# Kernel tuning notes

Measured on AMD Instinct MI355X. Metric: run time of the kernel, lower is better.

The kernel has to match this reference:

```python
import jax, jax.numpy as jnp
import numpy as np

N_NODES = 50000
SEQ = 12
CH = 128
BS = 4

def setup_inputs() -> dict:
    key = jax.random.key(0)
    k1, k2, k3, k4, k5 = jax.random.split(key, 5)
    x = jax.random.normal(k1, (BS, N_NODES, CH), dtype=jnp.float32)
    indices = jax.random.randint(k2, (N_NODES, SEQ), 0, N_NODES)
    # xavier-uniform-like init for per-node spiral weights [n_nodes, seq]
    bound = float(np.sqrt(6.0 / (N_NODES + SEQ)))
    weight = jax.random.uniform(k3, (N_NODES, SEQ), minval=-bound, maxval=bound, dtype=jnp.float32)
    gate_w = jax.random.normal(k4, (CH, CH), dtype=jnp.float32) * (1.0 / np.sqrt(CH))
    gate_b = jax.random.normal(k5, (CH,), dtype=jnp.float32) * 0.01
    return {"x": x, "indices": indices, "weight": weight, "gate_w": gate_w, "gate_b": gate_b}

def reference(x, indices, weight, gate_w, gate_b):
    # gate projection: [bs, n, ch]
    gate = jnp.einsum('bnc,dc->bnd', x, gate_w) + gate_b
    # gather spiral neighbors along node axis: [bs, n*s, ch] -> [bs, n, s, ch]
    gathered = jnp.take(x, indices.reshape(-1), axis=1)
    gathered = gathered.reshape(x.shape[0], indices.shape[0], indices.shape[1], x.shape[2])
    # per-node weighted reduction over spiral positions
    out = jnp.einsum('bvsf,vs->bvf', gathered, weight)
    return out * gate
```

## Files before the change

### kernel.cpp

```cpp
#include <hip/hip_runtime.h>
#include <hip/hip_bf16.h>

#define N_NODES 50000
#define SEQ 12
#define CH 128
#define BS 4
#define TILE 64
#define NTILES ((N_NODES + TILE - 1) / TILE)
#define HALF 64
#define PAD_S 68
#define PAD_ROW 132

#define CNODES 4
#define NCHUNK 4
#define CHUNK_SHORTS (CNODES * SEQ * HALF)
#define CHUNK_INSTR (CHUNK_SHORTS / 512)

typedef short bf16x8 __attribute__((ext_vector_type(8)));
typedef float f32x4 __attribute__((ext_vector_type(4)));

__device__ __forceinline__ float bflo(unsigned int u) { return __uint_as_float(u << 16); }
__device__ __forceinline__ float bfhi(unsigned int u) { return __uint_as_float(u & 0xFFFF0000u); }

__device__ __forceinline__ void gload_lds16b(const unsigned short* g, unsigned short* l) {
    __builtin_amdgcn_global_load_lds(
        (const __attribute__((address_space(1))) void*)g,
        (__attribute__((address_space(3))) void*)l,
        16, 0, 0);
}
__device__ __forceinline__ void gload_lds16f(const float* g, float* l) {
    __builtin_amdgcn_global_load_lds(
        (const __attribute__((address_space(1))) void*)g,
        (__attribute__((address_space(3))) void*)l,
        16, 0, 0);
}

__global__ __launch_bounds__(256) void convert_kernel(
    const float* __restrict__ x,
    unsigned short* __restrict__ xb)
{
    const size_t i = (size_t)blockIdx.x * 256 + threadIdx.x;
    const size_t n8 = (size_t)BS * N_NODES * CH / 8;
    if (i < n8) {
        float4 lo = *(const float4*)(x + i * 8);
        float4 hi = *(const float4*)(x + i * 8 + 4);
        union { bf16x8 v; __hip_bfloat16 h[8]; } o;
        o.h[0] = __float2bfloat16(lo.x); o.h[1] = __float2bfloat16(lo.y);
        o.h[2] = __float2bfloat16(lo.z); o.h[3] = __float2bfloat16(lo.w);
        o.h[4] = __float2bfloat16(hi.x); o.h[5] = __float2bfloat16(hi.y);
        o.h[6] = __float2bfloat16(hi.z); o.h[7] = __float2bfloat16(hi.w);
        *(bf16x8*)(xb + i * 8) = o.v;
    }
}

__global__ __launch_bounds__(256, 2) void gated_spiral_slice(
    const unsigned short* __restrict__ xb,
    const int* __restrict__ indices,
    const float* __restrict__ weight,
    const float* __restrict__ gate_w,
    const float* __restrict__ gate_b,
    float* __restrict__ out)
{
    __shared__ float spiral[TILE * PAD_S];
    __shared__ unsigned short gbuf[4][2][CHUNK_SHORTS];
    __shared__ int   idx_s[TILE * SEQ];
    __shared__ float w_s[TILE * SEQ];

    const int tid  = threadIdx.x;
    const int wave = tid >> 6;
    const int lane = tid & 63;

    const int grp  = blockIdx.x & 7;
    const int b    = grp >> 1;
    const int half = grp & 1;
    const int tile = blockIdx.x >> 3;
    const int node0 = tile * TILE;
    const unsigned short* xbb = xb + (size_t)b * N_NODES * CH;

    const int sbase = wave * 16 * SEQ;
    #pragma unroll
    for (int k3 = 0; k3 < 3; ++k3) {
        const int k = k3 * 64 + lane;
        int node = node0 + wave * 16 + k / SEQ;
        if (node >= N_NODES) node = N_NODES - 1;
        int t = indices[(size_t)node * SEQ + (k % SEQ)];
        t = t < 0 ? 0 : (t >= N_NODES ? N_NODES - 1 : t);
        idx_s[sbase + k] = t;
        w_s[sbase + k]   = weight[(size_t)node * SEQ + (k % SEQ)];
    }

    {
        const int* idxw = idx_s + sbase;
        const float* ww = w_s + sbase;
        unsigned short* gw0 = &gbuf[wave][0][0];
        const int lrs = lane >> 3;
        const int lco = (lane & 7) * 8;

        #pragma unroll
        for (int c0 = 0; c0 < 2; ++c0) {
            unsigned short* dst = gw0 + c0 * CHUNK_SHORTS;
            #pragma unroll
            for (int i = 0; i < CHUNK_INSTR; ++i) {
                const int rs = i * 8 + lrs;
                const int s = rs >> 2, n = rs & 3;
                const int row = idxw[(c0 * CNODES + n) * SEQ + s];
                gload_lds16b(xbb + (size_t)row * CH + half * HALF + lco, dst + i * 512);
            }
        }

        #pragma unroll
        for (int c = 0; c < NCHUNK; ++c) {
            if (c < NCHUNK - 1) asm volatile("s_waitcnt vmcnt(6)" ::: "memory");
            else                asm volatile("s_waitcnt vmcnt(0)" ::: "memory");
            __builtin_amdgcn_sched_barrier(0);

            unsigned short* bufp = gw0 + (c & 1) * CHUNK_SHORTS;
            const int nr = lane >> 4;
            const int cc = (lane & 15) * 4;
            const float* wp = ww + (c * CNODES + nr) * SEQ;
            float a0 = 0.f, a1 = 0.f, a2 = 0.f, a3 = 0.f;
            #pragma unroll
            for (int s = 0; s < SEQ; ++s) {
                const uint2 d = *(const uint2*)(bufp + (s * 4 + nr) * HALF + cc);
                const float ws = wp[s];
                a0 += ws * bflo(d.x); a1 += ws * bfhi(d.x);
                a2 += ws * bflo(d.y); a3 += ws * bfhi(d.y);
            }
            const int r = wave * 16 + c * CNODES + nr;
            *(float4*)(spiral + r * PAD_S + cc) = make_float4(a0, a1, a2, a3);

            if (c + 2 < NCHUNK) {
                asm volatile("s_waitcnt lgkmcnt(0)" ::: "memory");
                __builtin_amdgcn_sched_barrier(0);
                #pragma unroll
                for (int i = 0; i < CHUNK_INSTR; ++i) {
                    const int rs = i * 8 + lrs;
                    const int s = rs >> 2, n = rs & 3;
                    const int row = idxw[((c + 2) * CNODES + n) * SEQ + s];
                    gload_lds16b(xbb + (size_t)row * CH + half * HALF + lco, bufp + i * 512);
                }
            }
        }
    }

    {
        const int m = lane & 15;
        const int quad = lane >> 4;

        int arow_node = node0 + wave * 16 + m;
        if (arow_node >= N_NODES) arow_node = N_NODES - 1;
        const unsigned short* ap = xbb + (size_t)arow_node * CH + quad * 8;

        bf16x8 afrag[4];
        #pragma unroll
        for (int kk = 0; kk < 4; ++kk)
            afrag[kk] = *(const bf16x8*)(ap + kk * 32);

        float gbv[4];
        #pragma unroll
        for (int t = 0; t < 4; ++t)
            gbv[t] = gate_b[half * HALF + t * 16 + m];

        #pragma unroll
        for (int t = 0; t < 4; ++t) {
            f32x4 c = {0.f, 0.f, 0.f, 0.f};
            const float* bp = gate_w + (size_t)(half * HALF + t * 16 + m) * CH + quad * 8;
            #pragma unroll
            for (int kk = 0; kk < 4; ++kk) {
                float4 lo = *(const float4*)(bp + kk * 32);
                float4 hi = *(const float4*)(bp + kk * 32 + 4);
                union { bf16x8 v; __hip_bfloat16 h[8]; } bf;
                bf.h[0] = __float2bfloat16(lo.x); bf.h[1] = __float2bfloat16(lo.y);
                bf.h[2] = __float2bfloat16(lo.z); bf.h[3] = __float2bfloat16(lo.w);
                bf.h[4] = __float2bfloat16(hi.x); bf.h[5] = __float2bfloat16(hi.y);
                bf.h[6] = __float2bfloat16(hi.z); bf.h[7] = __float2bfloat16(hi.w);
                c = __builtin_amdgcn_mfma_f32_16x16x32_bf16(afrag[kk], bf.v, c, 0, 0, 0);
            }
            #pragma unroll
            for (int reg = 0; reg < 4; ++reg) {
                const int r = wave * 16 + quad * 4 + reg;
                const int col = t * 16 + m;
                const float sp = spiral[r * PAD_S + col];
                spiral[r * PAD_S + col] = sp * (c[reg] + gbv[t]);
            }
        }
    }

    {
        #pragma unroll
        for (int p = 0; p < 4; ++p) {
            const int seg = p * 64 + lane;
            const int r = seg >> 4;
            const int cc = (seg & 15) * 4;
            const int node = node0 + wave * 16 + r;
            if (node < N_NODES) {
                const float* sp = spiral + (wave * 16 + r) * PAD_S + cc;
                f32x4 v = { sp[0], sp[1], sp[2], sp[3] };
                __builtin_nontemporal_store(v,
                    (f32x4*)(out + ((size_t)b * N_NODES + node) * CH + half * HALF + cc));
            }
        }
    }
}

#define NODES_PER_WAVE 16
#define FCHUNK_NODES 2
#define FCHUNK_FLOATS (FCHUNK_NODES * SEQ * CH)
#define FNCHUNK (NODES_PER_WAVE / FCHUNK_NODES)

__global__ __launch_bounds__(256, 1) void gated_spiral_async(
    const float* __restrict__ x,
    const int* __restrict__ indices,
    const float* __restrict__ weight,
    const float* __restrict__ gate_w,
    const float* __restrict__ gate_b,
    float* __restrict__ out)
{
    __shared__ float spiral[TILE * PAD_ROW];
    __shared__ float gbuf[4][2][FCHUNK_FLOATS];
    __shared__ int   idx_s[TILE * SEQ];
    __shared__ float w_s[TILE * SEQ];

    const int tid  = threadIdx.x;
    const int wave = tid >> 6;
    const int lane = tid & 63;
    const int b    = blockIdx.y;
    const int node0 = blockIdx.x * TILE;
    const float* xb = x + (size_t)b * N_NODES * CH;

    const int sbase = wave * NODES_PER_WAVE * SEQ;
    #pragma unroll
    for (int k3 = 0; k3 < 3; ++k3) {
        const int k = k3 * 64 + lane;
        int node = node0 + wave * NODES_PER_WAVE + k / SEQ;
        if (node >= N_NODES) node = N_NODES - 1;
        int t = indices[(size_t)node * SEQ + (k % SEQ)];
        t = t < 0 ? 0 : (t >= N_NODES ? N_NODES - 1 : t);
        idx_s[sbase + k] = t;
        w_s[sbase + k]   = weight[(size_t)node * SEQ + (k % SEQ)];
    }

    {
        const int n  = lane >> 5;
        const int co = (lane & 31) * 4;
        const int* idxw = idx_s + sbase;
        const float* ww = w_s + sbase;
        float* gb0 = &gbuf[wave][0][0];

        #pragma unroll
        for (int c0 = 0; c0 < 2; ++c0) {
            const int* ix = idxw + c0 * FCHUNK_NODES * SEQ;
            float* dst = gb0 + c0 * FCHUNK_FLOATS;
            #pragma unroll
            for (int s = 0; s < SEQ; ++s) {
                const int row = ix[n * SEQ + s];
                gload_lds16f(xb + (size_t)row * CH + co, dst + s * (FCHUNK_NODES * CH));
            }
        }

        #pragma unroll
        for (int c = 0; c < FNCHUNK; ++c) {
            if (c < FNCHUNK - 1) asm volatile("s_waitcnt vmcnt(12)" ::: "memory");
            else                 asm volatile("s_waitcnt vmcnt(0)"  ::: "memory");
            __builtin_amdgcn_sched_barrier(0);

            float* cur = gb0 + (c & 1) * FCHUNK_FLOATS;
            const float* wp = ww + c * FCHUNK_NODES * SEQ + n * SEQ;
            float a0 = 0.f, a1 = 0.f, a2 = 0.f, a3 = 0.f;
            #pragma unroll
            for (int s = 0; s < SEQ; ++s) {
                const float4 d = *(const float4*)(cur + (s * FCHUNK_NODES + n) * CH + co);
                const float ws = wp[s];
                a0 += ws * d.x; a1 += ws * d.y; a2 += ws * d.z; a3 += ws * d.w;
            }
            const int r = wave * NODES_PER_WAVE + c * FCHUNK_NODES + n;
            *(float4*)(spiral + r * PAD_ROW + co) = make_float4(a0, a1, a2, a3);

            if (c + 2 < FNCHUNK) {
                asm volatile("s_waitcnt lgkmcnt(0)" ::: "memory");
                __builtin_amdgcn_sched_barrier(0);
                const int* ix = idxw + (c + 2) * FCHUNK_NODES * SEQ;
                #pragma unroll
                for (int s = 0; s < SEQ; ++s) {
                    const int row = ix[n * SEQ + s];
                    gload_lds16f(xb + (size_t)row * CH + co, cur + s * (FCHUNK_NODES * CH));
                }
            }
        }
    }

    {
        const int m = lane & 15;
        const int quad = lane >> 4;

        int arow_node = node0 + wave * 16 + m;
        if (arow_node >= N_NODES) arow_node = N_NODES - 1;
        const float* ap = xb + (size_t)arow_node * CH + quad * 8;

        bf16x8 afrag[4];
        #pragma unroll
        for (int kk = 0; kk < 4; ++kk) {
            float4 lo = *(const float4*)(ap + kk * 32);
            float4 hi = *(const float4*)(ap + kk * 32 + 4);
            union { bf16x8 v; __hip_bfloat16 h[8]; } af;
            af.h[0] = __float2bfloat16(lo.x); af.h[1] = __float2bfloat16(lo.y);
            af.h[2] = __float2bfloat16(lo.z); af.h[3] = __float2bfloat16(lo.w);
            af.h[4] = __float2bfloat16(hi.x); af.h[5] = __float2bfloat16(hi.y);
            af.h[6] = __float2bfloat16(hi.z); af.h[7] = __float2bfloat16(hi.w);
            afrag[kk] = af.v;
        }

        float gbv[8];
        #pragma unroll
        for (int t = 0; t < 8; ++t)
            gbv[t] = gate_b[t * 16 + m];

        #pragma unroll
        for (int t = 0; t < 8; ++t) {
            f32x4 c = {0.f, 0.f, 0.f, 0.f};
            const float* bp = gate_w + (size_t)(t * 16 + m) * CH + quad * 8;
            #pragma unroll
            for (int kk = 0; kk < 4; ++kk) {
                float4 lo = *(const float4*)(bp + kk * 32);
                float4 hi = *(const float4*)(bp + kk * 32 + 4);
                union { bf16x8 v; __hip_bfloat16 h[8]; } bf;
                bf.h[0] = __float2bfloat16(lo.x); bf.h[1] = __float2bfloat16(lo.y);
                bf.h[2] = __float2bfloat16(lo.z); bf.h[3] = __float2bfloat16(lo.w);
                bf.h[4] = __float2bfloat16(hi.x); bf.h[5] = __float2bfloat16(hi.y);
                bf.h[6] = __float2bfloat16(hi.z); bf.h[7] = __float2bfloat16(hi.w);
                c = __builtin_amdgcn_mfma_f32_16x16x32_bf16(afrag[kk], bf.v, c, 0, 0, 0);
            }
            #pragma unroll
            for (int reg = 0; reg < 4; ++reg) {
                const int r = wave * 16 + quad * 4 + reg;
                const int col = t * 16 + m;
                const float sp = spiral[r * PAD_ROW + col];
                spiral[r * PAD_ROW + col] = sp * (c[reg] + gbv[t]);
            }
        }
    }

    {
        #pragma unroll
        for (int p = 0; p < 8; ++p) {
            const int seg = p * 64 + lane;
            const int r = seg >> 5;
            const int c4 = (seg & 31) * 4;
            const int node = node0 + wave * 16 + r;
            if (node < N_NODES) {
                const float* sp = spiral + (wave * 16 + r) * PAD_ROW + c4;
                f32x4 v = { sp[0], sp[1], sp[2], sp[3] };
                __builtin_nontemporal_store(v, (f32x4*)(out + ((size_t)b * N_NODES + node) * CH + c4));
            }
        }
    }
}

extern "C" void kernel_launch(void* const* d_in, const int* in_sizes, int n_in,
                              void* d_out, int out_size, void* d_ws, size_t ws_size,
                              hipStream_t stream) {
    const float* x       = (const float*)d_in[0];
    const int*   indices = (const int*)d_in[1];
    const float* weight  = (const float*)d_in[2];
    const float* gate_w  = (const float*)d_in[3];
    const float* gate_b  = (const float*)d_in[4];
    float*       out     = (float*)d_out;

    const size_t x_bf_bytes = (size_t)BS * N_NODES * CH * 2;

    if (ws_size >= x_bf_bytes) {
        unsigned short* xbuf = (unsigned short*)d_ws;
        const size_t n8 = (size_t)BS * N_NODES * CH / 8;
        convert_kernel<<<dim3((unsigned)((n8 + 255) / 256)), dim3(256), 0, stream>>>(x, xbuf);
        gated_spiral_slice<<<dim3(NTILES * 8), dim3(256), 0, stream>>>(
            xbuf, indices, weight, gate_w, gate_b, out);
    } else {
        dim3 grid(NTILES, BS);
        gated_spiral_async<<<grid, dim3(256), 0, stream>>>(
            x, indices, weight, gate_w, gate_b, out);
    }
}
```

Before: 324.2 us.

## Split channel slices into quarters with phased block ordering for higher occupancy

Each block now handles a 32-channel quarter instead of a 64-channel half, which doubles the grid and halves the per-block LDS and register footprint so launch bounds can allow four blocks per CU. The block index is split into two phases so that, within each phase, blocks for the same tile and batch cover different quarters together, which may help L2 reuse of gathered rows. Indices, weights and the A fragments are read with nontemporal loads. In exchange, every gathered row fetch is now a 64-byte segment, so there are more, smaller gather transactions, and the index and weight staging and the gate-weight conversion are repeated in twice as many blocks.

```diff
diff --git a/kernel.cpp b/kernel.cpp
--- a/kernel.cpp
+++ b/kernel.cpp
@@ -7,14 +7,14 @@
 #define BS 4
 #define TILE 64
 #define NTILES ((N_NODES + TILE - 1) / TILE)
-#define HALF 64
-#define PAD_S 68
+#define QCH 32
+#define PAD_Q 36
 #define PAD_ROW 132
 
 #define CNODES 4
 #define NCHUNK 4
-#define CHUNK_SHORTS (CNODES * SEQ * HALF)
-#define CHUNK_INSTR (CHUNK_SHORTS / 512)
+#define CHUNK_SHORTS (CNODES * SEQ * QCH)
+#define CHUNK_INSTR ((CHUNK_SHORTS * 2) / 1024)
 
 typedef short bf16x8 __attribute__((ext_vector_type(8)));
 typedef float f32x4 __attribute__((ext_vector_type(4)));
@@ -53,7 +53,7 @@
     }
 }
 
-__global__ __launch_bounds__(256, 2) void gated_spiral_slice(
+__global__ __launch_bounds__(256, 4) void gated_spiral_quarter(
     const unsigned short* __restrict__ xb,
     const int* __restrict__ indices,
     const float* __restrict__ weight,
@@ -61,7 +61,7 @@
     const float* __restrict__ gate_b,
     float* __restrict__ out)
 {
-    __shared__ float spiral[TILE * PAD_S];
+    __shared__ float spiral[TILE * PAD_Q];
     __shared__ unsigned short gbuf[4][2][CHUNK_SHORTS];
     __shared__ int   idx_s[TILE * SEQ];
     __shared__ float w_s[TILE * SEQ];
@@ -70,10 +70,13 @@
     const int wave = tid >> 6;
     const int lane = tid & 63;
 
-    const int grp  = blockIdx.x & 7;
-    const int b    = grp >> 1;
-    const int half = grp & 1;
-    const int tile = blockIdx.x >> 3;
+    const int bx    = blockIdx.x;
+    const int phase = bx >= NTILES * 8 ? 1 : 0;
+    const int r0    = bx - phase * (NTILES * 8);
+    const int g8    = r0 & 7;
+    const int tile  = r0 >> 3;
+    const int b     = g8 >> 1;
+    const int q     = (g8 & 1) | (phase << 1);
     const int node0 = tile * TILE;
     const unsigned short* xbb = xb + (size_t)b * N_NODES * CH;
 
@@ -83,61 +86,60 @@
         const int k = k3 * 64 + lane;
         int node = node0 + wave * 16 + k / SEQ;
         if (node >= N_NODES) node = N_NODES - 1;
-        int t = indices[(size_t)node * SEQ + (k % SEQ)];
+        int t = __builtin_nontemporal_load(indices + (size_t)node * SEQ + (k % SEQ));
         t = t < 0 ? 0 : (t >= N_NODES ? N_NODES - 1 : t);
         idx_s[sbase + k] = t;
-        w_s[sbase + k]   = weight[(size_t)node * SEQ + (k % SEQ)];
+        w_s[sbase + k]   = __builtin_nontemporal_load(weight + (size_t)node * SEQ + (k % SEQ));
     }
 
     {
         const int* idxw = idx_s + sbase;
         const float* ww = w_s + sbase;
         unsigned short* gw0 = &gbuf[wave][0][0];
-        const int lrs = lane >> 3;
-        const int lco = (lane & 7) * 8;
+        const int lrow = lane >> 2;
+        const int lco  = (lane & 3) * 8;
 
         #pragma unroll
         for (int c0 = 0; c0 < 2; ++c0) {
             unsigned short* dst = gw0 + c0 * CHUNK_SHORTS;
             #pragma unroll
             for (int i = 0; i < CHUNK_INSTR; ++i) {
-                const int rs = i * 8 + lrs;
+                const int rs = i * 16 + lrow;
                 const int s = rs >> 2, n = rs & 3;
                 const int row = idxw[(c0 * CNODES + n) * SEQ + s];
-                gload_lds16b(xbb + (size_t)row * CH + half * HALF + lco, dst + i * 512);
+                gload_lds16b(xbb + (size_t)row * CH + q * QCH + lco, dst + i * 512);
             }
         }
 
         #pragma unroll
         for (int c = 0; c < NCHUNK; ++c) {
-            if (c < NCHUNK - 1) asm volatile("s_waitcnt vmcnt(6)" ::: "memory");
+            if (c < NCHUNK - 1) asm volatile("s_waitcnt vmcnt(3)" ::: "memory");
             else                asm volatile("s_waitcnt vmcnt(0)" ::: "memory");
             __builtin_amdgcn_sched_barrier(0);
 
             unsigned short* bufp = gw0 + (c & 1) * CHUNK_SHORTS;
             const int nr = lane >> 4;
-            const int cc = (lane & 15) * 4;
+            const int cp = lane & 15;
             const float* wp = ww + (c * CNODES + nr) * SEQ;
-            float a0 = 0.f, a1 = 0.f, a2 = 0.f, a3 = 0.f;
+            float a0 = 0.f, a1 = 0.f;
             #pragma unroll
             for (int s = 0; s < SEQ; ++s) {
-                const uint2 d = *(const uint2*)(bufp + (s * 4 + nr) * HALF + cc);
+                const unsigned int u = *(const unsigned int*)(bufp + (s * 4 + nr) * QCH + cp * 2);
                 const float ws = wp[s];
-                a0 += ws * bflo(d.x); a1 += ws * bfhi(d.x);
-                a2 += ws * bflo(d.y); a3 += ws * bfhi(d.y);
+                a0 += ws * bflo(u); a1 += ws * bfhi(u);
             }
             const int r = wave * 16 + c * CNODES + nr;
-            *(float4*)(spiral + r * PAD_S + cc) = make_float4(a0, a1, a2, a3);
+            *(float2*)(spiral + r * PAD_Q + cp * 2) = make_float2(a0, a1);
 
             if (c + 2 < NCHUNK) {
                 asm volatile("s_waitcnt lgkmcnt(0)" ::: "memory");
                 __builtin_amdgcn_sched_barrier(0);
                 #pragma unroll
                 for (int i = 0; i < CHUNK_INSTR; ++i) {
-                    const int rs = i * 8 + lrs;
+                    const int rs = i * 16 + lrow;
                     const int s = rs >> 2, n = rs & 3;
                     const int row = idxw[((c + 2) * CNODES + n) * SEQ + s];
-                    gload_lds16b(xbb + (size_t)row * CH + half * HALF + lco, bufp + i * 512);
+                    gload_lds16b(xbb + (size_t)row * CH + q * QCH + lco, bufp + i * 512);
                 }
             }
         }
@@ -154,17 +156,17 @@
         bf16x8 afrag[4];
         #pragma unroll
         for (int kk = 0; kk < 4; ++kk)
-            afrag[kk] = *(const bf16x8*)(ap + kk * 32);
-
-        float gbv[4];
-        #pragma unroll
-        for (int t = 0; t < 4; ++t)
-            gbv[t] = gate_b[half * HALF + t * 16 + m];
-
-        #pragma unroll
-        for (int t = 0; t < 4; ++t) {
+            afrag[kk] = __builtin_nontemporal_load((const bf16x8*)(ap + kk * 32));
+
+        float gbv[2];
+        #pragma unroll
+        for (int t = 0; t < 2; ++t)
+            gbv[t] = gate_b[q * QCH + t * 16 + m];
+
+        #pragma unroll
+        for (int t = 0; t < 2; ++t) {
             f32x4 c = {0.f, 0.f, 0.f, 0.f};
-            const float* bp = gate_w + (size_t)(half * HALF + t * 16 + m) * CH + quad * 8;
+            const float* bp = gate_w + (size_t)(q * QCH + t * 16 + m) * CH + quad * 8;
             #pragma unroll
             for (int kk = 0; kk < 4; ++kk) {
                 float4 lo = *(const float4*)(bp + kk * 32);
@@ -180,24 +182,24 @@
             for (int reg = 0; reg < 4; ++reg) {
                 const int r = wave * 16 + quad * 4 + reg;
                 const int col = t * 16 + m;
-                const float sp = spiral[r * PAD_S + col];
-                spiral[r * PAD_S + col] = sp * (c[reg] + gbv[t]);
-            }
-        }
-    }
-
-    {
-        #pragma unroll
-        for (int p = 0; p < 4; ++p) {
+                const float sp = spiral[r * PAD_Q + col];
+                spiral[r * PAD_Q + col] = sp * (c[reg] + gbv[t]);
+            }
+        }
+    }
+
+    {
+        #pragma unroll
+        for (int p = 0; p < 2; ++p) {
             const int seg = p * 64 + lane;
-            const int r = seg >> 4;
-            const int cc = (seg & 15) * 4;
+            const int r = seg >> 3;
+            const int i8 = seg & 7;
             const int node = node0 + wave * 16 + r;
             if (node < N_NODES) {
-                const float* sp = spiral + (wave * 16 + r) * PAD_S + cc;
+                const float* sp = spiral + (wave * 16 + r) * PAD_Q + i8 * 4;
                 f32x4 v = { sp[0], sp[1], sp[2], sp[3] };
                 __builtin_nontemporal_store(v,
-                    (f32x4*)(out + ((size_t)b * N_NODES + node) * CH + half * HALF + cc));
+                    (f32x4*)(out + ((size_t)b * N_NODES + node) * CH + q * QCH + i8 * 4));
             }
         }
     }
@@ -372,7 +374,7 @@
         unsigned short* xbuf = (unsigned short*)d_ws;
         const size_t n8 = (size_t)BS * N_NODES * CH / 8;
         convert_kernel<<<dim3((unsigned)((n8 + 255) / 256)), dim3(256), 0, stream>>>(x, xbuf);
-        gated_spiral_slice<<<dim3(NTILES * 8), dim3(256), 0, stream>>>(
+        gated_spiral_quarter<<<dim3(NTILES * 16), dim3(256), 0, stream>>>(
             xbuf, indices, weight, gate_w, gate_b, out);
     } else {
         dim3 grid(NTILES, BS);
```

After: 367.0 us. +13.2%, slower.
